# Kernel optimization log

Measured on AMD Instinct MI355X. Metric: run time of the kernel, lower is better.

Reference implementation:

```python
import jax, jax.numpy as jnp
import numpy as np

B = 2048
N_USERS = 100000
N_ITEMS = 50000
N = N_USERS + N_ITEMS
EMB = 64
NNZ = 100000


def setup_inputs() -> dict:
    key = jax.random.key(0)
    k1, k2, k3, k4 = jax.random.split(key, 4)
    u_id = jax.random.randint(k1, (B,), 0, N_USERS, dtype=jnp.int64 if jax.config.jax_enable_x64 else jnp.int32)
    pos_i_id = jax.random.randint(k2, (B,), 0, N, dtype=u_id.dtype)
    train_mask = jax.random.randint(k3, (2, NNZ), 0, B, dtype=u_id.dtype)
    all_embed = jax.random.normal(k4, (N, EMB), dtype=jnp.float32)
    return {"u_id": u_id, "pos_i_id": pos_i_id, "train_mask": train_mask, "all_embed": all_embed}


def reference(u_id, pos_i_id, train_mask, all_embed):
    # policy_type == 'uij': scores = (u_e + pos_e) @ all_e^T  -> [B, N]
    u_e = all_embed[u_id]
    pos_e = all_embed[pos_i_id]
    scores = jnp.einsum("bd,nd->bn", u_e + pos_e, all_embed)
    # Note: the original computes a sparse train-mask tensor (sp_mask) but never
    # uses it; only the zero->-inf masking below affects the output.
    logits = jnp.where(scores == 0.0, -jnp.inf, scores)
    probs = jax.nn.softmax(logits, axis=1)  # [B, N]
    # Categorical sampling per row (fixed key for reproducibility)
    samples = jax.random.categorical(jax.random.key(42), logits, axis=1)  # [B]
    selected_neg_prob = jnp.take_along_axis(probs, samples[:, None], axis=1)[:, 0]
    return samples, selected_neg_prob
```

## Files before the change

kernel.cpp:

```cpp
#include <hip/hip_runtime.h>
#include <stdint.h>

#define B_ROWS   2048
#define N_COLS   150000
#define NSTRIPS  128
#define CHUNK    128
#define NCHUNK   1172
#define ROWG     16

#define NEG_HUGE (-3.0e38f)
#define G_SPAN_HARD  20.6f
#define G_MAX_MARGIN 15.944f
#define EPS_B        2.0e-4f
#define G_FILTER_SLACK 3e-5f
#define DEFER_THR_LOG2 12.0f

#define LOG2E_F 1.44269504088896340736f
#define LN2_F   0.69314718055994530942f

#if __has_builtin(__builtin_amdgcn_exp2f)
#define EXP2F(x) __builtin_amdgcn_exp2f(x)
#else
#define EXP2F(x) exp2f(x)
#endif

#define WS_MPART 0
#define WS_ZPART (B_ROWS * NSTRIPS)
#define WS_CMAX  (2 * B_ROWS * NSTRIPS)
#define WS_M     (WS_CMAX + B_ROWS * NCHUNK)
#define WS_Z     (WS_M + B_ROWS)
#define WS_VLB   (WS_Z + B_ROWS)
#define WS_CSTAR (WS_VLB + B_ROWS)
#define WS_BEST  (WS_CSTAR + B_ROWS)
#define WS_ENORM (WS_BEST + 2 * B_ROWS)
#define WS_QNORM (WS_ENORM + 2048)
#define WS_EHI   (WS_QNORM + B_ROWS)
#define WS_ELO   (WS_EHI + NCHUNK * 4096)
#define WS_END   (WS_ELO + NCHUNK * 4096)

typedef __attribute__((ext_vector_type(8))) unsigned short ushort8;
typedef __attribute__((ext_vector_type(8))) short short8;
typedef __attribute__((ext_vector_type(4))) float f32x4;

__device__ __forceinline__ uint32_t rotl32(uint32_t x, int r) {
  return (x << r) | (x >> (32 - r));
}

__device__ __forceinline__ void threefry2x32_k42(uint32_t& x0, uint32_t& x1) {
  const uint32_t ks0 = 0u;
  const uint32_t ks1 = 42u;
  const uint32_t ks2 = 0x1BD11BDAu ^ 0u ^ 42u;
  x0 += ks0; x1 += ks1;
#define TF_R(r) { x0 += x1; x1 = rotl32(x1, (r)); x1 ^= x0; }
  TF_R(13) TF_R(15) TF_R(26) TF_R(6)
  x0 += ks1; x1 += ks2 + 1u;
  TF_R(17) TF_R(29) TF_R(16) TF_R(24)
  x0 += ks2; x1 += ks0 + 2u;
  TF_R(13) TF_R(15) TF_R(26) TF_R(6)
  x0 += ks0; x1 += ks1 + 3u;
  TF_R(17) TF_R(29) TF_R(16) TF_R(24)
  x0 += ks1; x1 += ks2 + 4u;
  TF_R(13) TF_R(15) TF_R(26) TF_R(6)
  x0 += ks2; x1 += ks0 + 5u;
#undef TF_R
}

__device__ __forceinline__ float gumbel_from_bits(uint32_t bits) {
  const uint32_t mant = bits >> 9;
  const float f = __uint_as_float(mant | 0x3f800000u) - 1.0f;
  const float l1 = mant ? log1pf(f - 1.0f) : -87.33654475055311f;
  return -__logf(-l1);
}

__device__ __forceinline__ float gumbel_at(uint32_t flat_idx) {
  uint32_t x0 = 0u, x1 = flat_idx;
  threefry2x32_k42(x0, x1);
  return gumbel_from_bits(x0 ^ x1);
}

__device__ __forceinline__ unsigned long long pack_vn(float v, int n) {
  uint32_t u = __float_as_uint(v);
  u ^= ((uint32_t)((int32_t)u >> 31)) | 0x80000000u;
  return ((unsigned long long)u << 32) | (uint32_t)(0xFFFFFFFFu - (uint32_t)n);
}

__device__ __forceinline__ float unpack_v(unsigned long long p) {
  uint32_t u = (uint32_t)(p >> 32);
  u = (u & 0x80000000u) ? (u ^ 0x80000000u) : ~u;
  return __uint_as_float(u);
}

__device__ __forceinline__ int unpack_n(unsigned long long p) {
  return (int)(0xFFFFFFFFu - (uint32_t)(p & 0xFFFFFFFFull));
}

__device__ __forceinline__ unsigned long long umax64(unsigned long long a,
                                                     unsigned long long b) {
  return a > b ? a : b;
}

__device__ __forceinline__ float dot_q_e(const float4* q4, const float4* e4) {
  float s = 0.0f;
#pragma unroll
  for (int k4 = 0; k4 < 16; ++k4) {
    const float4 e = e4[k4];
    const float4 q = q4[k4];
    s = fmaf(q.x, e.x, s);
    s = fmaf(q.y, e.y, s);
    s = fmaf(q.z, e.z, s);
    s = fmaf(q.w, e.w, s);
  }
  return s;
}

__device__ __forceinline__ unsigned short f32_to_bf16_rne(float f) {
  const uint32_t u = __float_as_uint(f);
  return (unsigned short)((u + 0x7fffu + ((u >> 16) & 1u)) >> 16);
}
__device__ __forceinline__ float bf16_to_f32(unsigned short h) {
  return __uint_as_float(((uint32_t)h) << 16);
}

__global__ __launch_bounds__(256) void advnet_enorm(const float* __restrict__ emb,
                                                    float* __restrict__ ws) {
  const int c = blockIdx.x;
  const int t = threadIdx.x;
  const int lane = t & 63;
  const int row = t >> 1;
  const int n = c * CHUNK + row;
  float ss = 0.0f;
  if (n < N_COLS) {
    const float4* p = (const float4*)emb + (size_t)n * 16 + (t & 1) * 8;
#pragma unroll
    for (int i = 0; i < 8; ++i) {
      const float4 v = p[i];
      ss = fmaf(v.x, v.x, ss); ss = fmaf(v.y, v.y, ss);
      ss = fmaf(v.z, v.z, ss); ss = fmaf(v.w, v.w, ss);
    }
  }
  ss += __shfl_xor(ss, 1, 64);
  float mx = ss;
  for (int off = 2; off < 64; off <<= 1) mx = fmaxf(mx, __shfl_xor(mx, off, 64));
  __shared__ float sm[4];
  if (lane == 0) sm[t >> 6] = mx;
  __syncthreads();
  if (t == 0)
    ws[WS_ENORM + c] =
        sqrtf(fmaxf(fmaxf(sm[0], sm[1]), fmaxf(sm[2], sm[3]))) * 1.00002f;
}

__global__ __launch_bounds__(256) void advnet_ebuild(const float* __restrict__ emb,
                                                     float* __restrict__ ws) {
  const int c = blockIdx.x;
  const int t = threadIdx.x;
  char* hi_b = (char*)(ws + WS_EHI) + (size_t)c * 16384;
  char* lo_b = (char*)(ws + WS_ELO) + (size_t)c * 16384;
  float mx = 0.0f;
#pragma unroll
  for (int k = 0; k < 4; ++k) {
    const int j = t + 256 * k;
    const int row = j >> 3, kq = j & 7;
    const int n = c * CHUNK + row;
    ushort8 hi = (ushort8)0, lo = (ushort8)0;
    float ss = 0.0f;
    if (n < N_COLS) {
      const float4* ep = (const float4*)emb + (size_t)n * 16 + kq * 2;
      const float4 a0 = ep[0], a1 = ep[1];
      const float e[8] = {a0.x, a0.y, a0.z, a0.w, a1.x, a1.y, a1.z, a1.w};
#pragma unroll
      for (int j8 = 0; j8 < 8; ++j8) {
        const unsigned short h = f32_to_bf16_rne(e[j8]);
        hi[j8] = h;
        lo[j8] = f32_to_bf16_rne(e[j8] - bf16_to_f32(h));
        ss = fmaf(e[j8], e[j8], ss);
      }
    }
    const int gz = kq ^ (row & 7);
    *(ushort8*)(hi_b + (size_t)(row * 8 + gz) * 16) = hi;
    *(ushort8*)(lo_b + (size_t)(row * 8 + gz) * 16) = lo;
    ss += __shfl_xor(ss, 1, 64);
    ss += __shfl_xor(ss, 2, 64);
    ss += __shfl_xor(ss, 4, 64);
    mx = fmaxf(mx, ss);
  }
  for (int off = 8; off < 64; off <<= 1) mx = fmaxf(mx, __shfl_xor(mx, off, 64));
  __shared__ float sm[4];
  if ((t & 63) == 0) sm[t >> 6] = mx;
  __syncthreads();
  if (t == 0)
    ws[WS_ENORM + c] =
        sqrtf(fmaxf(fmaxf(sm[0], sm[1]), fmaxf(sm[2], sm[3]))) * 1.00002f;
}

__device__ __forceinline__ void stage_tbl(const char* tb_hi, const char* tb_lo,
                                          unsigned short* eh, unsigned short* el,
                                          int c, int wave, int lane) {
  const size_t cb = (size_t)c * 16384 + (size_t)(wave * 1024 + lane * 16);
  const int wo = wave * 1024;
#pragma unroll
  for (int i = 0; i < 4; ++i) {
    const int off = i * 4096;
    __builtin_amdgcn_global_load_lds(
        (const __attribute__((address_space(1))) void*)(tb_hi + cb + off),
        (__attribute__((address_space(3))) void*)((char*)eh + wo + off), 16, 0, 0);
    __builtin_amdgcn_global_load_lds(
        (const __attribute__((address_space(1))) void*)(tb_lo + cb + off),
        (__attribute__((address_space(3))) void*)((char*)el + wo + off), 16, 0, 0);
  }
}

__device__ __forceinline__ void stage_conv(const float* __restrict__ emb,
                                           unsigned short* eh, unsigned short* el,
                                           int c, int tid) {
  const int n0 = c * CHUNK;
#pragma unroll
  for (int k = 0; k < 4; ++k) {
    const int p = tid + 256 * k;
    const int row = p >> 3, kq = p & 7;
    const int n = n0 + row;
    ushort8 hi = (ushort8)0, lo = (ushort8)0;
    if (n < N_COLS) {
      const float4* ep = (const float4*)emb + (size_t)n * 16 + kq * 2;
      const float4 a0 = ep[0], a1 = ep[1];
      const float e[8] = {a0.x, a0.y, a0.z, a0.w, a1.x, a1.y, a1.z, a1.w};
#pragma unroll
      for (int j = 0; j < 8; ++j) {
        const unsigned short h = f32_to_bf16_rne(e[j]);
        hi[j] = h;
        lo[j] = f32_to_bf16_rne(e[j] - bf16_to_f32(h));
      }
    }
    const int off = row * 64 + ((kq * 8) ^ ((row & 7) << 3));
    *(ushort8*)&eh[off] = hi;
    *(ushort8*)&el[off] = lo;
  }
}

template <bool TBL>
__global__ __launch_bounds__(256, 2) void advnet_gemm(
    const int* __restrict__ u_id, const int* __restrict__ pos_id,
    const float* __restrict__ emb, float* __restrict__ ws) {
  __shared__ unsigned short eh_s[8192], el_s[8192];

  const int tid = threadIdx.x;
  const int raw = blockIdx.x;
  const int b8 = raw & 7;
  const int rest = raw >> 3;
  const int rg = rest & 15;
  const int strip = b8 + 8 * (rest >> 4);
  const int wave = tid >> 6;
  const int lane = tid & 63;
  const int lc = lane & 15;
  const int lg = lane >> 4;

#pragma unroll
  for (int k = 0; k < 4; ++k) {
    const int p = tid + 256 * k;
    const int row = p >> 3, kq = p & 7;
    const int b = rg * 128 + row;
    const float4* ua = (const float4*)emb + (size_t)u_id[b] * 16 + kq * 2;
    const float4* pa = (const float4*)emb + (size_t)pos_id[b] * 16 + kq * 2;
    const float4 a0 = ua[0], a1 = ua[1], c0 = pa[0], c1 = pa[1];
    const float q[8] = {(a0.x + c0.x) * LOG2E_F, (a0.y + c0.y) * LOG2E_F,
                        (a0.z + c0.z) * LOG2E_F, (a0.w + c0.w) * LOG2E_F,
                        (a1.x + c1.x) * LOG2E_F, (a1.y + c1.y) * LOG2E_F,
                        (a1.z + c1.z) * LOG2E_F, (a1.w + c1.w) * LOG2E_F};
    ushort8 hi, lo;
#pragma unroll
    for (int j = 0; j < 8; ++j) {
      const unsigned short h = f32_to_bf16_rne(q[j]);
      hi[j] = h;
      lo[j] = f32_to_bf16_rne(q[j] - bf16_to_f32(h));
    }
    const int off = row * 64 + ((kq * 8) ^ ((row & 7) << 3));
    *(ushort8*)&eh_s[off] = hi;
    *(ushort8*)&el_s[off] = lo;
  }
  __syncthreads();

  short8 qh_r[2][2], ql_r[2][2];
#pragma unroll
  for (int kh = 0; kh < 2; ++kh)
#pragma unroll
    for (int rt = 0; rt < 2; ++rt) {
      const int r = wave * 32 + rt * 16 + lc;
      const int off = r * 64 + (((kh * 4 + lg) * 8) ^ ((r & 7) << 3));
      qh_r[kh][rt] = *(const short8*)&eh_s[off];
      ql_r[kh][rt] = *(const short8*)&el_s[off];
    }
  __syncthreads();

  float m[8], Z[8];
#pragma unroll
  for (int s = 0; s < 8; ++s) { m[s] = NEG_HUGE; Z[s] = 0.0f; }

  const char* tb_hi = (const char*)(ws + WS_EHI);
  const char* tb_lo = (const char*)(ws + WS_ELO);

  for (int c = strip; c < NCHUNK; c += NSTRIPS) {
    if (TBL) stage_tbl(tb_hi, tb_lo, eh_s, el_s, c, wave, lane);
    else     stage_conv(emb, eh_s, el_s, c, tid);
    __syncthreads();

    f32x4 acc[2][8];
#pragma unroll
    for (int rt = 0; rt < 2; ++rt)
#pragma unroll
      for (int ct = 0; ct < 8; ++ct) acc[rt][ct] = (f32x4){0.f, 0.f, 0.f, 0.f};

#pragma unroll
    for (int kh = 0; kh < 2; ++kh) {
#pragma unroll
      for (int ct = 0; ct < 8; ++ct) {
        const int col = ct * 16 + lc;
        const int off = col * 64 + (((kh * 4 + lg) * 8) ^ ((col & 7) << 3));
        const short8 ehf = *(const short8*)&eh_s[off];
        const short8 elf = *(const short8*)&el_s[off];
#pragma unroll
        for (int rt = 0; rt < 2; ++rt) {
          acc[rt][ct] = __builtin_amdgcn_mfma_f32_16x16x32_bf16(qh_r[kh][rt], ehf, acc[rt][ct], 0, 0, 0);
          acc[rt][ct] = __builtin_amdgcn_mfma_f32_16x16x32_bf16(qh_r[kh][rt], elf, acc[rt][ct], 0, 0, 0);
          acc[rt][ct] = __builtin_amdgcn_mfma_f32_16x16x32_bf16(ql_r[kh][rt], ehf, acc[rt][ct], 0, 0, 0);
        }
      }
    }

#pragma unroll
    for (int rt = 0; rt < 2; ++rt) {
#pragma unroll
      for (int j = 0; j < 4; ++j) {
        const int s = rt * 4 + j;
        float cm = acc[rt][0][j];
#pragma unroll
        for (int ct = 1; ct < 8; ++ct) cm = fmaxf(cm, acc[rt][ct][j]);
        if (cm > m[s] + DEFER_THR_LOG2) {
          Z[s] *= EXP2F(m[s] - cm);
          m[s] = cm;
        }
        float za = 0.0f;
#pragma unroll
        for (int ct = 0; ct < 8; ++ct) za += EXP2F(acc[rt][ct][j] - m[s]);
        Z[s] += za;
        float cr = cm;
        cr = fmaxf(cr, __shfl_xor(cr, 1, 64));
        cr = fmaxf(cr, __shfl_xor(cr, 2, 64));
        cr = fmaxf(cr, __shfl_xor(cr, 4, 64));
        cr = fmaxf(cr, __shfl_xor(cr, 8, 64));
        if (lc == 0) {
          const int row = rg * 128 + wave * 32 + rt * 16 + lg * 4 + j;
          ws[WS_CMAX + (size_t)row * NCHUNK + c] = cr;
        }
      }
    }
    __syncthreads();
  }

#pragma unroll
  for (int rt = 0; rt < 2; ++rt) {
#pragma unroll
    for (int j = 0; j < 4; ++j) {
      const int s = rt * 4 + j;
      float mi = m[s], Zi = Z[s];
      for (int off = 1; off < 16; off <<= 1) {
        const float om = __shfl_xor(mi, off, 64);
        const float oZ = __shfl_xor(Zi, off, 64);
        const float nm = fmaxf(mi, om);
        Zi = Zi * EXP2F(mi - nm) + oZ * EXP2F(om - nm);
        mi = nm;
      }
      if (lc == 0) {
        const int row = rg * 128 + wave * 32 + rt * 16 + lg * 4 + j;
        ws[WS_MPART + (size_t)row * NSTRIPS + strip] = mi;
        ws[WS_ZPART + (size_t)row * NSTRIPS + strip] = Zi;
      }
    }
  }
}

__global__ __launch_bounds__(128) void advnet_rowstat(
    const int* __restrict__ u_id, const int* __restrict__ pos_id,
    const float* __restrict__ emb, float* __restrict__ ws) {
  const int r = blockIdx.x;
  const int t = threadIdx.x;

  __shared__ float sA[2], sB[2];
  __shared__ unsigned long long sP[2];
  __shared__ float qrow[64];

  const size_t idx = (size_t)r * NSTRIPS + t;
  const float ms = ws[WS_MPART + idx];
  const float zs = ws[WS_ZPART + idx];
  float Ms = ms;
  for (int off = 1; off < 64; off <<= 1) Ms = fmaxf(Ms, __shfl_xor(Ms, off, 64));
  if ((t & 63) == 0) sA[t >> 6] = Ms;
  __syncthreads();
  Ms = fmaxf(sA[0], sA[1]);
  float z = zs * EXP2F(ms - Ms);
  for (int off = 1; off < 64; off <<= 1) z += __shfl_xor(z, off, 64);
  if ((t & 63) == 0) sB[t >> 6] = z;
  __syncthreads();
  const float Z = sB[0] + sB[1];
  const float M_nat = Ms * LN2_F;

  unsigned long long cp = 0ull;
  for (int c = t; c < NCHUNK; c += 128)
    cp = umax64(cp, pack_vn(ws[WS_CMAX + (size_t)r * NCHUNK + c], c));
  for (int off = 1; off < 64; off <<= 1)
    cp = umax64(cp, __shfl_xor(cp, off, 64));
  if ((t & 63) == 0) sP[t >> 6] = cp;
  __syncthreads();
  cp = umax64(sP[0], sP[1]);
  const int cstar = unpack_n(cp);

  if (t < 16) {
    const float4 a = ((const float4*)emb)[(size_t)u_id[r] * 16 + t];
    const float4 c = ((const float4*)emb)[(size_t)pos_id[r] * 16 + t];
    ((float4*)qrow)[t] = make_float4(a.x + c.x, a.y + c.y, a.z + c.z, a.w + c.w);
  }
  __syncthreads();

  {
    const float qv = qrow[t & 63];
    float ss = qv * qv;
    for (int off = 1; off < 64; off <<= 1) ss += __shfl_xor(ss, off, 64);
    if (t == 0) ws[WS_QNORM + r] = sqrtf(ss) * 1.00002f;
  }

  unsigned long long bp = 0ull;
  const int n = cstar * CHUNK + t;
  if (n < N_COLS) {
    const float s = dot_q_e((const float4*)qrow, (const float4*)emb + (size_t)n * 16);
    if (s != 0.0f && s >= M_nat - G_SPAN_HARD) {
      const uint32_t L = (uint32_t)r * (uint32_t)N_COLS + (uint32_t)n;
      bp = pack_vn(gumbel_at(L) + s, n);
    }
  }
  for (int off = 1; off < 64; off <<= 1)
    bp = umax64(bp, __shfl_xor(bp, off, 64));
  if ((t & 63) == 0) sP[t >> 6] = bp;
  __syncthreads();
  if (t == 0) {
    const unsigned long long best = umax64(sP[0], sP[1]);
    ((unsigned long long*)(ws + WS_BEST))[r] = best;
    ws[WS_VLB + r] = unpack_v(best);
    ws[WS_M + r] = M_nat;
    ws[WS_Z + r] = Z;
    ((int*)ws)[WS_CSTAR + r] = cstar;
  }
}

#define SVCAP 2048
__global__ __launch_bounds__(256) void advnet_pick(
    const int* __restrict__ u_id, const int* __restrict__ pos_id,
    const float* __restrict__ emb, float* __restrict__ ws) {
  const int r = blockIdx.x >> 1;
  const int par = blockIdx.x & 1;
  const int t = threadIdx.x;

  __shared__ float qrow[64];
  __shared__ unsigned short cq[600];
  __shared__ float cqg[600];
  __shared__ unsigned int svpk[SVCAP];
  __shared__ float svg[SVCAP];
  __shared__ int cqn, svn;
  __shared__ unsigned long long sred[4];

  if (t == 0) { cqn = 0; svn = 0; }
  if (t < 16) {
    const float4 a = ((const float4*)emb)[(size_t)u_id[r] * 16 + t];
    const float4 c = ((const float4*)emb)[(size_t)pos_id[r] * 16 + t];
    ((float4*)qrow)[t] = make_float4(a.x + c.x, a.y + c.y, a.z + c.z, a.w + c.w);
  }
  const float vlb = ws[WS_VLB + r];
  const float bq = ws[WS_QNORM + r] * EPS_B;
  const int cstar = ((const int*)ws)[WS_CSTAR + r];
  __syncthreads();

  for (int c = par + 2 * t; c < NCHUNK; c += 512) {
    if (c == cstar) continue;
    const float cm = ws[WS_CMAX + (size_t)r * NCHUNK + c];
    const float gth = vlb - fmaf(cm, LN2_F, bq * ws[WS_ENORM + c]);
    if (gth < G_MAX_MARGIN) {
      const int k = atomicAdd(&cqn, 1);
      cq[k] = (unsigned short)c;
      cqg[k] = gth;
    }
  }
  __syncthreads();
  const int nq = cqn;
  const float4* qr4 = (const float4*)qrow;

  unsigned long long bp = 0ull;

  for (int base = 0; base < nq; base += 8) {
    if (svn > SVCAP - 1024) {
      __syncthreads();
      const int cnt = svn;
      for (int k = t; k < cnt; k += 256) {
        const int n = (int)svpk[k];
        const float s = dot_q_e(qr4, (const float4*)emb + (size_t)n * 16);
        if (s != 0.0f) bp = umax64(bp, pack_vn(svg[k] + s, n));
      }
      __syncthreads();
      if (t == 0) svn = 0;
      __syncthreads();
    }
#pragma unroll
    for (int u = 0; u < 4; ++u) {
      const int idx = t + 256 * u;
      const int slot = base + (idx >> 7);
      if (slot < nq) {
        const int n = (int)cq[slot] * CHUNK + (idx & 127);
        if (n < N_COLS) {
          const float g = gumbel_at((uint32_t)r * (uint32_t)N_COLS + (uint32_t)n);
          if (g > cqg[slot] - G_FILTER_SLACK) {
            const int k = atomicAdd(&svn, 1);
            if (k < SVCAP) { svpk[k] = (unsigned)n; svg[k] = g; }
          }
        }
      }
    }
    __syncthreads();
  }

  {
    const int cnt = svn < SVCAP ? svn : SVCAP;
    for (int k = t; k < cnt; k += 256) {
      const int n = (int)svpk[k];
      const float s = dot_q_e(qr4, (const float4*)emb + (size_t)n * 16);
      if (s != 0.0f) bp = umax64(bp, pack_vn(svg[k] + s, n));
    }
  }

  for (int off = 1; off < 64; off <<= 1)
    bp = umax64(bp, __shfl_xor(bp, off, 64));
  if ((t & 63) == 0) sred[t >> 6] = bp;
  __syncthreads();
  if (t == 0) {
    const unsigned long long b =
        umax64(umax64(sred[0], sred[1]), umax64(sred[2], sred[3]));
    if (b) atomicMax((unsigned long long*)(ws + WS_BEST) + r, b);
  }
}

__global__ __launch_bounds__(64) void advnet_final(
    const int* __restrict__ u_id, const int* __restrict__ pos_id,
    const float* __restrict__ emb, const float* __restrict__ ws,
    float* __restrict__ out) {
  const int r = blockIdx.x * 64 + threadIdx.x;
  if (r >= B_ROWS) return;
  const unsigned long long w = ((const unsigned long long*)(ws + WS_BEST))[r];
  const int n = unpack_n(w);
  const float4* qa = (const float4*)emb + (size_t)u_id[r] * 16;
  const float4* qb = (const float4*)emb + (size_t)pos_id[r] * 16;
  const float4* e4 = (const float4*)emb + (size_t)n * 16;
  float s = 0.0f;
#pragma unroll
  for (int k4 = 0; k4 < 16; ++k4) {
    const float4 a = qa[k4], b = qb[k4], e = e4[k4];
    float4 q;
    q.x = a.x + b.x; q.y = a.y + b.y; q.z = a.z + b.z; q.w = a.w + b.w;
    s = fmaf(q.x, e.x, s);
    s = fmaf(q.y, e.y, s);
    s = fmaf(q.z, e.z, s);
    s = fmaf(q.w, e.w, s);
  }
  out[r] = (float)n;
  out[B_ROWS + r] = __expf(s - ws[WS_M + r]) / ws[WS_Z + r];
}

extern "C" void kernel_launch(void* const* d_in, const int* in_sizes, int n_in,
                              void* d_out, int out_size, void* d_ws, size_t ws_size,
                              hipStream_t stream) {
  const int* u_id = (const int*)d_in[0];
  const int* pos_id = (const int*)d_in[1];
  const float* emb = (const float*)d_in[3];
  float* ws = (float*)d_ws;
  float* out = (float*)d_out;

  const size_t need = (size_t)WS_END * 4;
  const bool tbl = ws_size >= need;

  if (tbl) {
    advnet_ebuild<<<dim3(NCHUNK), dim3(256), 0, stream>>>(emb, ws);
    advnet_gemm<true><<<dim3(ROWG * NSTRIPS), dim3(256), 0, stream>>>(
        u_id, pos_id, emb, ws);
  } else {
    advnet_enorm<<<dim3(NCHUNK), dim3(256), 0, stream>>>(emb, ws);
    advnet_gemm<false><<<dim3(ROWG * NSTRIPS), dim3(256), 0, stream>>>(
        u_id, pos_id, emb, ws);
  }
  advnet_rowstat<<<dim3(B_ROWS), dim3(128), 0, stream>>>(u_id, pos_id, emb, ws);
  advnet_pick<<<dim3(B_ROWS * 2), dim3(256), 0, stream>>>(u_id, pos_id, emb, ws);
  advnet_final<<<dim3(B_ROWS / 64), dim3(64), 0, stream>>>(u_id, pos_id, emb, ws, out);
}
```

Measured before the change: 259.0 us.

## Split chunk staging into halves and double-buffer LDS to overlap loads with MFMA

Each 128-column chunk is split into two 64-column halves held in two LDS buffers. While one half is multiplied with MFMA and fed to the online softmax, the next half (or the first half of the next chunk) is staged, so global loads overlap compute instead of being serialized before a barrier. The per-chunk column max is now gathered across both halves in a separate accumulator. Total LDS use is unchanged, but the half-size tiles give fewer MFMAs per barrier and the ping-pong indexing is more complex.

```diff
diff --git a/kernel.cpp b/kernel.cpp
--- a/kernel.cpp
+++ b/kernel.cpp
@@ -192,13 +192,14 @@
         sqrtf(fmaxf(fmaxf(sm[0], sm[1]), fmaxf(sm[2], sm[3]))) * 1.00002f;
 }
 
-__device__ __forceinline__ void stage_tbl(const char* tb_hi, const char* tb_lo,
-                                          unsigned short* eh, unsigned short* el,
-                                          int c, int wave, int lane) {
-  const size_t cb = (size_t)c * 16384 + (size_t)(wave * 1024 + lane * 16);
+__device__ __forceinline__ void stage_tbl_half(const char* tb_hi, const char* tb_lo,
+                                               unsigned short* eh, unsigned short* el,
+                                               int c, int h, int wave, int lane) {
+  const size_t cb = (size_t)c * 16384 + (size_t)(h * 8192) +
+                    (size_t)(wave * 1024 + lane * 16);
   const int wo = wave * 1024;
 #pragma unroll
-  for (int i = 0; i < 4; ++i) {
+  for (int i = 0; i < 2; ++i) {
     const int off = i * 4096;
     __builtin_amdgcn_global_load_lds(
         (const __attribute__((address_space(1))) void*)(tb_hi + cb + off),
@@ -209,12 +210,12 @@
   }
 }
 
-__device__ __forceinline__ void stage_conv(const float* __restrict__ emb,
-                                           unsigned short* eh, unsigned short* el,
-                                           int c, int tid) {
-  const int n0 = c * CHUNK;
-#pragma unroll
-  for (int k = 0; k < 4; ++k) {
+__device__ __forceinline__ void stage_conv_half(const float* __restrict__ emb,
+                                                unsigned short* eh, unsigned short* el,
+                                                int c, int h, int tid) {
+  const int n0 = c * CHUNK + h * 64;
+#pragma unroll
+  for (int k = 0; k < 2; ++k) {
     const int p = tid + 256 * k;
     const int row = p >> 3, kq = p & 7;
     const int n = n0 + row;
@@ -225,14 +226,62 @@
       const float e[8] = {a0.x, a0.y, a0.z, a0.w, a1.x, a1.y, a1.z, a1.w};
 #pragma unroll
       for (int j = 0; j < 8; ++j) {
-        const unsigned short h = f32_to_bf16_rne(e[j]);
-        hi[j] = h;
-        lo[j] = f32_to_bf16_rne(e[j] - bf16_to_f32(h));
+        const unsigned short h2 = f32_to_bf16_rne(e[j]);
+        hi[j] = h2;
+        lo[j] = f32_to_bf16_rne(e[j] - bf16_to_f32(h2));
       }
     }
     const int off = row * 64 + ((kq * 8) ^ ((row & 7) << 3));
     *(ushort8*)&eh[off] = hi;
     *(ushort8*)&el[off] = lo;
+  }
+}
+
+__device__ __forceinline__ void gemm_half(
+    const unsigned short* EH, const unsigned short* EL,
+    const short8 qh_r[2][2], const short8 ql_r[2][2],
+    int lc, int lg, float m[8], float Z[8], float cmh[8]) {
+  f32x4 acc[2][4];
+#pragma unroll
+  for (int rt = 0; rt < 2; ++rt)
+#pragma unroll
+    for (int ct = 0; ct < 4; ++ct) acc[rt][ct] = (f32x4){0.f, 0.f, 0.f, 0.f};
+
+#pragma unroll
+  for (int kh = 0; kh < 2; ++kh) {
+#pragma unroll
+    for (int ct = 0; ct < 4; ++ct) {
+      const int l = ct * 16 + lc;
+      const int off = l * 64 + (((kh * 4 + lg) * 8) ^ ((l & 7) << 3));
+      const short8 ehf = *(const short8*)&EH[off];
+      const short8 elf = *(const short8*)&EL[off];
+#pragma unroll
+      for (int rt = 0; rt < 2; ++rt) {
+        acc[rt][ct] = __builtin_amdgcn_mfma_f32_16x16x32_bf16(qh_r[kh][rt], ehf, acc[rt][ct], 0, 0, 0);
+        acc[rt][ct] = __builtin_amdgcn_mfma_f32_16x16x32_bf16(qh_r[kh][rt], elf, acc[rt][ct], 0, 0, 0);
+        acc[rt][ct] = __builtin_amdgcn_mfma_f32_16x16x32_bf16(ql_r[kh][rt], ehf, acc[rt][ct], 0, 0, 0);
+      }
+    }
+  }
+
+#pragma unroll
+  for (int rt = 0; rt < 2; ++rt) {
+#pragma unroll
+    for (int j = 0; j < 4; ++j) {
+      const int s = rt * 4 + j;
+      float cm = acc[rt][0][j];
+#pragma unroll
+      for (int ct = 1; ct < 4; ++ct) cm = fmaxf(cm, acc[rt][ct][j]);
+      cmh[s] = fmaxf(cmh[s], cm);
+      if (cm > m[s] + DEFER_THR_LOG2) {
+        Z[s] *= EXP2F(m[s] - cm);
+        m[s] = cm;
+      }
+      float za = 0.0f;
+#pragma unroll
+      for (int ct = 0; ct < 4; ++ct) za += EXP2F(acc[rt][ct][j] - m[s]);
+      Z[s] += za;
+    }
   }
 }
 
@@ -240,7 +289,7 @@
 __global__ __launch_bounds__(256, 2) void advnet_gemm(
     const int* __restrict__ u_id, const int* __restrict__ pos_id,
     const float* __restrict__ emb, float* __restrict__ ws) {
-  __shared__ unsigned short eh_s[8192], el_s[8192];
+  __shared__ unsigned short eh0[4096], el0[4096], eh1[4096], el1[4096];
 
   const int tid = threadIdx.x;
   const int raw = blockIdx.x;
@@ -272,9 +321,12 @@
       hi[j] = h;
       lo[j] = f32_to_bf16_rne(q[j] - bf16_to_f32(h));
     }
-    const int off = row * 64 + ((kq * 8) ^ ((row & 7) << 3));
-    *(ushort8*)&eh_s[off] = hi;
-    *(ushort8*)&el_s[off] = lo;
+    unsigned short* EH = (k < 2) ? eh0 : eh1;
+    unsigned short* EL = (k < 2) ? el0 : el1;
+    const int rl = row & 63;
+    const int off = rl * 64 + ((kq * 8) ^ ((rl & 7) << 3));
+    *(ushort8*)&EH[off] = hi;
+    *(ushort8*)&EL[off] = lo;
   }
   __syncthreads();
 
@@ -284,64 +336,56 @@
 #pragma unroll
     for (int rt = 0; rt < 2; ++rt) {
       const int r = wave * 32 + rt * 16 + lc;
-      const int off = r * 64 + (((kh * 4 + lg) * 8) ^ ((r & 7) << 3));
-      qh_r[kh][rt] = *(const short8*)&eh_s[off];
-      ql_r[kh][rt] = *(const short8*)&el_s[off];
-    }
-  __syncthreads();
-
-  float m[8], Z[8];
-#pragma unroll
-  for (int s = 0; s < 8; ++s) { m[s] = NEG_HUGE; Z[s] = 0.0f; }
+      const unsigned short* EH = (wave < 2) ? eh0 : eh1;
+      const unsigned short* EL = (wave < 2) ? el0 : el1;
+      const int rl = r & 63;
+      const int off = rl * 64 + (((kh * 4 + lg) * 8) ^ ((rl & 7) << 3));
+      qh_r[kh][rt] = *(const short8*)&EH[off];
+      ql_r[kh][rt] = *(const short8*)&EL[off];
+    }
+  __syncthreads();
+
+  float m[8], Z[8], cmh[8];
+#pragma unroll
+  for (int s = 0; s < 8; ++s) { m[s] = NEG_HUGE; Z[s] = 0.0f; cmh[s] = NEG_HUGE; }
 
   const char* tb_hi = (const char*)(ws + WS_EHI);
   const char* tb_lo = (const char*)(ws + WS_ELO);
 
+  if (TBL) stage_tbl_half(tb_hi, tb_lo, eh0, el0, strip, 0, wave, lane);
+  else     stage_conv_half(emb, eh0, el0, strip, 0, tid);
+  __syncthreads();
+
+  int cur = 0;
   for (int c = strip; c < NCHUNK; c += NSTRIPS) {
-    if (TBL) stage_tbl(tb_hi, tb_lo, eh_s, el_s, c, wave, lane);
-    else     stage_conv(emb, eh_s, el_s, c, tid);
+    {
+      unsigned short* SEH = cur ? eh0 : eh1;
+      unsigned short* SEL = cur ? el0 : el1;
+      if (TBL) stage_tbl_half(tb_hi, tb_lo, SEH, SEL, c, 1, wave, lane);
+      else     stage_conv_half(emb, SEH, SEL, c, 1, tid);
+      const unsigned short* CEH = cur ? eh1 : eh0;
+      const unsigned short* CEL = cur ? el1 : el0;
+      gemm_half(CEH, CEL, qh_r, ql_r, lc, lg, m, Z, cmh);
+    }
     __syncthreads();
-
-    f32x4 acc[2][8];
-#pragma unroll
-    for (int rt = 0; rt < 2; ++rt)
-#pragma unroll
-      for (int ct = 0; ct < 8; ++ct) acc[rt][ct] = (f32x4){0.f, 0.f, 0.f, 0.f};
-
-#pragma unroll
-    for (int kh = 0; kh < 2; ++kh) {
-#pragma unroll
-      for (int ct = 0; ct < 8; ++ct) {
-        const int col = ct * 16 + lc;
-        const int off = col * 64 + (((kh * 4 + lg) * 8) ^ ((col & 7) << 3));
-        const short8 ehf = *(const short8*)&eh_s[off];
-        const short8 elf = *(const short8*)&el_s[off];
-#pragma unroll
-        for (int rt = 0; rt < 2; ++rt) {
-          acc[rt][ct] = __builtin_amdgcn_mfma_f32_16x16x32_bf16(qh_r[kh][rt], ehf, acc[rt][ct], 0, 0, 0);
-          acc[rt][ct] = __builtin_amdgcn_mfma_f32_16x16x32_bf16(qh_r[kh][rt], elf, acc[rt][ct], 0, 0, 0);
-          acc[rt][ct] = __builtin_amdgcn_mfma_f32_16x16x32_bf16(ql_r[kh][rt], ehf, acc[rt][ct], 0, 0, 0);
-        }
-      }
-    }
-
+    cur ^= 1;
+    {
+      if (c + NSTRIPS < NCHUNK) {
+        unsigned short* SEH = cur ? eh0 : eh1;
+        unsigned short* SEL = cur ? el0 : el1;
+        if (TBL) stage_tbl_half(tb_hi, tb_lo, SEH, SEL, c + NSTRIPS, 0, wave, lane);
+        else     stage_conv_half(emb, SEH, SEL, c + NSTRIPS, 0, tid);
+      }
+      const unsigned short* CEH = cur ? eh1 : eh0;
+      const unsigned short* CEL = cur ? el1 : el0;
+      gemm_half(CEH, CEL, qh_r, ql_r, lc, lg, m, Z, cmh);
+    }
 #pragma unroll
     for (int rt = 0; rt < 2; ++rt) {
 #pragma unroll
       for (int j = 0; j < 4; ++j) {
         const int s = rt * 4 + j;
-        float cm = acc[rt][0][j];
-#pragma unroll
-        for (int ct = 1; ct < 8; ++ct) cm = fmaxf(cm, acc[rt][ct][j]);
-        if (cm > m[s] + DEFER_THR_LOG2) {
-          Z[s] *= EXP2F(m[s] - cm);
-          m[s] = cm;
-        }
-        float za = 0.0f;
-#pragma unroll
-        for (int ct = 0; ct < 8; ++ct) za += EXP2F(acc[rt][ct][j] - m[s]);
-        Z[s] += za;
-        float cr = cm;
+        float cr = cmh[s];
         cr = fmaxf(cr, __shfl_xor(cr, 1, 64));
         cr = fmaxf(cr, __shfl_xor(cr, 2, 64));
         cr = fmaxf(cr, __shfl_xor(cr, 4, 64));
@@ -350,9 +394,11 @@
           const int row = rg * 128 + wave * 32 + rt * 16 + lg * 4 + j;
           ws[WS_CMAX + (size_t)row * NCHUNK + c] = cr;
         }
+        cmh[s] = NEG_HUGE;
       }
     }
     __syncthreads();
+    cur ^= 1;
   }
 
 #pragma unroll
```

Result: slower. 269.1 us (+3.9%).
